# Performance work log

Measured on AMD Instinct MI355X. Metric: run time of the kernel, lower is better.

Reference implementation:

```python
import jax, jax.numpy as jnp
import numpy as np

BETA = 0.25


def setup_inputs() -> dict:
    key = jax.random.key(0)
    k1, k2 = jax.random.split(key)
    x = jax.random.normal(k1, (32, 512, 32, 32), dtype=jnp.float32)
    # torchhd Random embedding: random bipolar {-1,+1} hypervectors, non-trainable
    codebook = jnp.sign(jax.random.normal(k2, (1024, 512), dtype=jnp.float32))
    codebook = jnp.where(codebook == 0, 1.0, codebook)
    return {"x": x, "codebook": codebook}


def reference(x, codebook):
    B, C, W, H = x.shape
    K = codebook.shape[0]
    # training-mode path: sharp sigmoid soft-binarization -> [-1, 1]
    xs = jax.nn.sigmoid(x * 100.0) * 2.0 - 1.0
    # [B, C, W, H] -> [B*W*H, C]
    flat = jnp.transpose(xs, (0, 2, 3, 1)).reshape(-1, C)
    # squared-distance via norms + matmul (same expansion as the torch code)
    d = (
        jnp.sum(flat * flat, axis=1, keepdims=True)
        + jnp.sum(codebook * codebook, axis=1)
        - 2.0 * flat @ codebook.T
    )  # [N, K]
    indices = jnp.argmin(d, axis=1)  # [N]
    # perplexity from empirical code usage (unique+counts == bincount over present codes)
    counts = jnp.bincount(indices, length=K).astype(jnp.float32)
    n = jnp.asarray(indices.shape[0], dtype=jnp.float32)
    p = counts / n
    plogp = jnp.where(counts > 0, p * jnp.log(p), 0.0)
    entropy = -jnp.sum(plogp)
    perplexity = jnp.exp(entropy)
    perplexity_loss = 1.0 / perplexity
    loss = BETA * perplexity_loss
    # embedding gather + reshape back to [B, C, W, H]
    q = codebook[indices].reshape(B, W, H, C)
    q = jnp.transpose(q, (0, 3, 1, 2))
    # straight-through estimator
    quantized = xs + jax.lax.stop_gradient(q - xs)
    return quantized, perplexity_loss, loss
```

## Files before the change

### kernel.cpp

```cpp
#include <hip/hip_runtime.h>
#include <stdint.h>
#include <stddef.h>

#define CD 512
#define KC 1024
#define NR 32768

typedef __attribute__((ext_vector_type(8))) short short8_t;
typedef __attribute__((ext_vector_type(8))) __bf16 bf16x8_t;
typedef __attribute__((ext_vector_type(4))) float f32x4_t;

__device__ __forceinline__ uint16_t f2bf(float f) {
  uint32_t u = __float_as_uint(f);
  u += 0x7fffu + ((u >> 16) & 1u);
  return (uint16_t)(u >> 16);
}
__device__ __forceinline__ float bf2f(uint16_t h) {
  return __uint_as_float(((uint32_t)h) << 16);
}
__device__ __forceinline__ float soft_sign(float x) {
  float e = __expf(-100.0f * x);
  float s = __builtin_amdgcn_rcpf(1.0f + e);
  return fmaf(2.0f, s, -1.0f);
}

__global__ __launch_bounds__(256) void k_cb(const float* __restrict__ cb,
                                            uint16_t* __restrict__ cbb,
                                            uint32_t* __restrict__ pack) {
  int i = blockIdx.x * 256 + threadIdx.x;
  float v = cb[i];
  int k = i >> 9, c = i & 511;
  int cc = c & 63;
  int swz = ((((cc >> 3) ^ (k & 7)) << 3) | (cc & 7));
  cbb[((size_t)k << 9) + (c & ~63) + swz] = f2bf(v);
  unsigned long long m = __ballot(v > 0.0f);
  int lane = threadIdx.x & 63;
  if ((lane & 31) == 0) pack[((c >> 5) << 10) + k] = (uint32_t)(m >> (lane & 32));
}

__global__ __launch_bounds__(256) void k_prep(const float* __restrict__ x,
                                              uint16_t* __restrict__ xhi,
                                              uint16_t* __restrict__ xlo,
                                              float* __restrict__ srow) {
  __shared__ float lxs[64][129];
  int blk = blockIdx.x;
  int b = blk >> 3;
  int p0 = (blk & 7) << 7;
  int tid = threadIdx.x;
  int n0 = (b << 10) + p0;
  int oc = tid & 7, nr = tid >> 3;
  double sum[4] = {0.0, 0.0, 0.0, 0.0};
  const float* xb = x + (((size_t)b) << 19) + p0;

  for (int ch = 0; ch < 8; ++ch) {
    int c0 = ch << 6;
#pragma unroll
    for (int it = 0; it < 8; ++it) {
      int cr = (it << 3) + (tid >> 5);
      int q = tid & 31;
      const float4 v =
          *reinterpret_cast<const float4*>(xb + (((size_t)(c0 + cr)) << 10) + (q << 2));
      lxs[cr][(q << 2) + 0] = soft_sign(v.x);
      lxs[cr][(q << 2) + 1] = soft_sign(v.y);
      lxs[cr][(q << 2) + 2] = soft_sign(v.z);
      lxs[cr][(q << 2) + 3] = soft_sign(v.w);
    }
    __syncthreads();
#pragma unroll
    for (int it = 0; it < 4; ++it) {
      int r = (it << 5) + nr;
      int n = n0 + r;
      short8_t h8, l8;
      double ls = 0.0;
#pragma unroll
      for (int j = 0; j < 8; ++j) {
        float xs = lxs[(oc << 3) + j][r];
        uint16_t h = f2bf(xs);
        uint16_t l = f2bf(xs - bf2f(h));
        h8[j] = (short)h;
        l8[j] = (short)l;
        float sq = xs * xs;
        ls += (double)sq;
      }
      sum[it] += ls;
      size_t off = (((size_t)n) << 9) + (size_t)c0 + (size_t)(((oc ^ (n & 7)) << 3));
      *reinterpret_cast<short8_t*>(xhi + off) = h8;
      *reinterpret_cast<short8_t*>(xlo + off) = l8;
    }
    __syncthreads();
  }
#pragma unroll
  for (int it = 0; it < 4; ++it) {
    double s = sum[it];
#pragma unroll
    for (int m = 1; m < 8; m <<= 1) s += __shfl_xor(s, m);
    if (oc == 0) srow[n0 + (it << 5) + nr] = (float)s + 512.0f;
  }
}

__device__ __forceinline__ void gl_lds16(const uint16_t* g, uint16_t* l) {
  __builtin_amdgcn_global_load_lds((const uint32_t*)g, (uint32_t*)l, 16, 0, 0);
}

__global__ __launch_bounds__(512, 1) void k_gemm(
    const uint16_t* __restrict__ cbb, const uint16_t* __restrict__ xhi,
    const uint16_t* __restrict__ xlo, const float* __restrict__ srow,
    int* __restrict__ idx, int* __restrict__ counts) {
  extern __shared__ uint8_t smem[];
  uint16_t* lds = (uint16_t*)smem;

  int blk = blockIdx.x;
  int tid = threadIdx.x;
  int lane = tid & 63, wid = tid >> 6;
  int kg = wid >> 1, pg = wid & 1;
  int g = lane >> 4, r15 = lane & 15;
  int n0 = blk << 6;

  float s_p[2];
#pragma unroll
  for (int ac = 0; ac < 2; ++ac) s_p[ac] = srow[n0 + (pg << 5) + (ac << 4) + r15];

  float best_d[2];
  int best_k[2];
#pragma unroll
  for (int ac = 0; ac < 2; ++ac) { best_d[ac] = 3.4e38f; best_k[ac] = 0; }

  auto stageA = [&](int buf, int kt, int cc) {
    const uint16_t* base = cbb + ((size_t)(cc << 6)) + ((lane & 7) << 3);
    uint16_t* lb = lds + (buf << 13);
#pragma unroll
    for (int i = 0; i < 2; ++i) {
      int r = (wid << 1) + i;
      gl_lds16(base + (((size_t)((kt << 7) + (r << 3) + (lane >> 3))) << 9), lb + (r << 9));
    }
  };
  auto stageB = [&](int cc) {
#pragma unroll
    for (int t = 0; t < 2; ++t) {
      const uint16_t* src = t ? xlo : xhi;
      gl_lds16(src + (((size_t)(n0 + (wid << 3) + (lane >> 3))) << 9) + (cc << 6) +
                   ((lane & 7) << 3),
               lds + 16384 + (t << 15) + (cc << 12) + (wid << 9));
    }
  };

  f32x4_t acc[2][2];

  stageA(0, 0, 0);
  stageB(0);
  asm volatile("s_waitcnt vmcnt(0)" ::: "memory");
  __builtin_amdgcn_s_barrier();
  asm volatile("" ::: "memory");

  int cur = 0;
  for (int step = 0; step < 64; ++step) {
    int kt = step >> 3, cc = step & 7;
    if (cc == 0) {
#pragma unroll
      for (int i = 0; i < 2; ++i)
#pragma unroll
        for (int j = 0; j < 2; ++j) acc[i][j] = (f32x4_t){0.f, 0.f, 0.f, 0.f};
    }
    if (step < 7) stageB(step + 1);
    if (step < 63) {
      int ns = step + 1;
      stageA(cur ^ 1, ns >> 3, ns & 7);
    }

    const uint16_t* Acur = lds + (cur << 13);
    const uint16_t* Bc = lds + 16384 + (cc << 12);
#pragma unroll
    for (int cs = 0; cs < 2; ++cs) {
      bf16x8_t af[2], bh[2], bl[2];
#pragma unroll
      for (int ar = 0; ar < 2; ++ar) {
        int row = (kg << 5) + (ar << 4) + r15;
        int off = (row << 6) + (((((cs << 2) | g)) ^ (row & 7)) << 3);
        af[ar] = __builtin_bit_cast(bf16x8_t, *(const short8_t*)(Acur + off));
      }
#pragma unroll
      for (int ac = 0; ac < 2; ++ac) {
        int row = (pg << 5) + (ac << 4) + r15;
        int off = (row << 6) + ((((cs << 2) | g) ^ (row & 7)) << 3);
        bh[ac] = __builtin_bit_cast(bf16x8_t, *(const short8_t*)(Bc + off));
        bl[ac] = __builtin_bit_cast(bf16x8_t, *(const short8_t*)(Bc + 32768 + off));
      }
#pragma unroll
      for (int ar = 0; ar < 2; ++ar)
#pragma unroll
        for (int ac = 0; ac < 2; ++ac) {
          acc[ar][ac] =
              __builtin_amdgcn_mfma_f32_16x16x32_bf16(af[ar], bh[ac], acc[ar][ac], 0, 0, 0);
          acc[ar][ac] =
              __builtin_amdgcn_mfma_f32_16x16x32_bf16(af[ar], bl[ac], acc[ar][ac], 0, 0, 0);
        }
    }

    if (cc == 7) {
      int kbase = (kt << 7) + (kg << 5);
#pragma unroll
      for (int ar = 0; ar < 2; ++ar)
#pragma unroll
        for (int ac = 0; ac < 2; ++ac)
#pragma unroll
          for (int rg = 0; rg < 4; ++rg) {
            float d = fmaf(-2.0f, acc[ar][ac][rg], s_p[ac]);
            int kk = kbase + (ar << 4) + (g << 2) + rg;
            bool better = (d < best_d[ac]) || (d == best_d[ac] && kk < best_k[ac]);
            if (better) { best_d[ac] = d; best_k[ac] = kk; }
          }
    }

    asm volatile("s_waitcnt vmcnt(0)" ::: "memory");
    __builtin_amdgcn_s_barrier();
    asm volatile("" ::: "memory");
    cur ^= 1;
  }

  float rd0, rd1;
  int rk0, rk1;
  {
    float d = best_d[0];
    int k = best_k[0];
#pragma unroll
    for (int m = 16; m <= 32; m <<= 1) {
      float od = __shfl_xor(d, m);
      int ok = __shfl_xor(k, m);
      if (od < d || (od == d && ok < k)) { d = od; k = ok; }
    }
    rd0 = d; rk0 = k;
  }
  {
    float d = best_d[1];
    int k = best_k[1];
#pragma unroll
    for (int m = 16; m <= 32; m <<= 1) {
      float od = __shfl_xor(d, m);
      int ok = __shfl_xor(k, m);
      if (od < d || (od == d && ok < k)) { d = od; k = ok; }
    }
    rd1 = d; rk1 = k;
  }
  float* sd = (float*)smem;
  int* sk = (int*)(smem + 1024);
  __syncthreads();
  if (g < 2) {
    float dv = (g == 0) ? rd0 : rd1;
    int kv = (g == 0) ? rk0 : rk1;
    sd[(kg << 6) + (pg << 5) + (g << 4) + r15] = dv;
    sk[(kg << 6) + (pg << 5) + (g << 4) + r15] = kv;
  }
  __syncthreads();
  if (tid < 64) {
    float d0 = sd[tid];
    int k0 = sk[tid];
#pragma unroll
    for (int kgi = 1; kgi < 4; ++kgi) {
      float d1 = sd[(kgi << 6) + tid];
      int k1 = sk[(kgi << 6) + tid];
      if (d1 < d0 || (d1 == d0 && k1 < k0)) { d0 = d1; k0 = k1; }
    }
    idx[n0 + tid] = k0;
    atomicAdd(&counts[k0], 1);
  }
}

__global__ __launch_bounds__(256) void k_perp(const int* __restrict__ counts,
                                              float* __restrict__ out2) {
  int tid = threadIdx.x;
  float local = 0.0f;
  for (int i = tid; i < KC; i += 256) {
    int c = counts[i];
    if (c > 0) {
      float p = (float)c * (1.0f / 32768.0f);
      local += p * logf(p);
    }
  }
#pragma unroll
  for (int m = 1; m < 64; m <<= 1) local += __shfl_xor(local, m);
  __shared__ float wsum[4];
  if ((tid & 63) == 0) wsum[tid >> 6] = local;
  __syncthreads();
  if (tid == 0) {
    float entropy = -(wsum[0] + wsum[1] + wsum[2] + wsum[3]);
    float pl = 1.0f / expf(entropy);
    out2[0] = pl;
    out2[1] = 0.25f * pl;
  }
}

__global__ __launch_bounds__(256) void k_gather(const int* __restrict__ idx,
                                                const uint32_t* __restrict__ pack,
                                                float* __restrict__ out) {
  __shared__ uint32_t lp[16384];
  int tid = threadIdx.x;
#pragma unroll
  for (int i = 0; i < 16; ++i)
    reinterpret_cast<uint4*>(lp)[i * 256 + tid] =
        reinterpret_cast<const uint4*>(pack)[i * 256 + tid];
  __syncthreads();
  int base = blockIdx.x * 2048;
  for (int it = 0; it < 8; ++it) {
    int t = base + it * 256 + tid;
    int pq = t & 255;
    int c = (t >> 8) & 511;
    int b = t >> 17;
    int4 iv = reinterpret_cast<const int4*>(idx)[(b << 8) + pq];
    int cw = c >> 5, cbit = c & 31;
    float4 r;
    r.x = ((lp[(cw << 10) + iv.x] >> cbit) & 1) ? 1.0f : -1.0f;
    r.y = ((lp[(cw << 10) + iv.y] >> cbit) & 1) ? 1.0f : -1.0f;
    r.z = ((lp[(cw << 10) + iv.z] >> cbit) & 1) ? 1.0f : -1.0f;
    r.w = ((lp[(cw << 10) + iv.w] >> cbit) & 1) ? 1.0f : -1.0f;
    reinterpret_cast<float4*>(out)[t] = r;
  }
}

extern "C" void kernel_launch(void* const* d_in, const int* in_sizes, int n_in,
                              void* d_out, int out_size, void* d_ws, size_t ws_size,
                              hipStream_t stream) {
  (void)in_sizes; (void)n_in; (void)out_size;
  const float* x = (const float*)d_in[0];
  const float* cb = (const float*)d_in[1];
  float* out = (float*)d_out;

  uint8_t* ws = (uint8_t*)d_ws;
  uint16_t* cbb = (uint16_t*)ws;
  float* srow = (float*)(ws + 1048576);
  int* idx = (int*)(ws + 1048576 + 131072);
  int* counts = (int*)(ws + 1048576 + 131072 + 131072);
  uint32_t* pack = (uint32_t*)(ws + 1048576 + 131072 + 131072 + 4096);
  size_t small_end = 1048576 + 131072 + 131072 + 4096 + 65536;

  uint16_t *xhi, *xlo;
  if (ws_size >= small_end + (size_t)NR * CD * 2 * 2) {
    xhi = (uint16_t*)(ws + small_end);
    xlo = xhi + (size_t)NR * CD;
  } else {
    xhi = (uint16_t*)d_out;
    xlo = xhi + (size_t)NR * CD;
  }

  hipFuncSetAttribute((const void*)k_gemm, hipFuncAttributeMaxDynamicSharedMemorySize,
                      163840);

  k_cb<<<2048, 256, 0, stream>>>(cb, cbb, pack);
  k_prep<<<256, 256, 0, stream>>>(x, xhi, xlo, srow);
  hipMemsetAsync(counts, 0, 4096, stream);
  k_gemm<<<512, 512, 163840, stream>>>(cbb, xhi, xlo, srow, idx, counts);
  k_perp<<<1, 256, 0, stream>>>(counts, out + 16777216);
  k_gather<<<2048, 256, 0, stream>>>(idx, pack, out);
}
```

Baseline: 225.3 us.

## Fuse soft-sign preprocessing into GEMM kernel and retile codebook stages

```diff
diff --git a/kernel.cpp b/kernel.cpp
--- a/kernel.cpp
+++ b/kernel.cpp
@@ -29,177 +29,143 @@
                                             uint32_t* __restrict__ pack) {
   int i = blockIdx.x * 256 + threadIdx.x;
   float v = cb[i];
+  cbb[i] = f2bf(v);
   int k = i >> 9, c = i & 511;
-  int cc = c & 63;
-  int swz = ((((cc >> 3) ^ (k & 7)) << 3) | (cc & 7));
-  cbb[((size_t)k << 9) + (c & ~63) + swz] = f2bf(v);
   unsigned long long m = __ballot(v > 0.0f);
   int lane = threadIdx.x & 63;
   if ((lane & 31) == 0) pack[((c >> 5) << 10) + k] = (uint32_t)(m >> (lane & 32));
 }
 
-__global__ __launch_bounds__(256) void k_prep(const float* __restrict__ x,
-                                              uint16_t* __restrict__ xhi,
-                                              uint16_t* __restrict__ xlo,
-                                              float* __restrict__ srow) {
-  __shared__ float lxs[64][129];
-  int blk = blockIdx.x;
-  int b = blk >> 3;
-  int p0 = (blk & 7) << 7;
-  int tid = threadIdx.x;
-  int n0 = (b << 10) + p0;
-  int oc = tid & 7, nr = tid >> 3;
-  double sum[4] = {0.0, 0.0, 0.0, 0.0};
+__device__ __forceinline__ void gl_lds16(const uint16_t* g, uint16_t* l) {
+  __builtin_amdgcn_global_load_lds((const uint32_t*)g, (uint32_t*)l, 16, 0, 0);
+}
+
+__global__ __launch_bounds__(512, 1) void k_gemm(const uint16_t* __restrict__ cbb,
+                                                 const float* __restrict__ x,
+                                                 int* __restrict__ idx,
+                                                 int* __restrict__ counts) {
+  extern __shared__ uint8_t smem[];
+  uint16_t* lds = (uint16_t*)smem;
+
+  const int tid = threadIdx.x;
+  const int lane = tid & 63, wid = tid >> 6;
+  const int kg = wid >> 1, pg = wid & 1;
+  const int g = lane >> 4, r15 = lane & 15;
+  const int blk = blockIdx.x;
+  const int n0 = blk << 6;
+  const int b = blk >> 4, p0 = (blk & 15) << 6;
+
+  auto stageA = [&](int buf, int kt, int cc) {
+    uint16_t* dst = lds + (buf << 13);
+    const uint16_t* srcb = cbb + ((size_t)(kt << 8)) * 512 + (cc << 5);
+#pragma unroll
+    for (int i = 0; i < 2; ++i) {
+      int u = (i << 9) + tid;
+      gl_lds16(srcb + (size_t)(u >> 2) * 512 + ((u & 3) << 3), dst + (u << 3));
+    }
+  };
+  stageA(0, 0, 0);
+
+  float* raw = (float*)(smem + 16384);
   const float* xb = x + (((size_t)b) << 19) + p0;
-
+  const int fr = tid >> 3, foc = tid & 7;
+  double nsum = 0.0;
   for (int ch = 0; ch < 8; ++ch) {
     int c0 = ch << 6;
 #pragma unroll
-    for (int it = 0; it < 8; ++it) {
-      int cr = (it << 3) + (tid >> 5);
-      int q = tid & 31;
+    for (int it = 0; it < 2; ++it) {
+      int u = (it << 9) + tid;
+      int cr = u >> 4, q = u & 15;
       const float4 v =
-          *reinterpret_cast<const float4*>(xb + (((size_t)(c0 + cr)) << 10) + (q << 2));
-      lxs[cr][(q << 2) + 0] = soft_sign(v.x);
-      lxs[cr][(q << 2) + 1] = soft_sign(v.y);
-      lxs[cr][(q << 2) + 2] = soft_sign(v.z);
-      lxs[cr][(q << 2) + 3] = soft_sign(v.w);
+          *reinterpret_cast<const float4*>(xb + (size_t)(c0 + cr) * 1024 + (q << 2));
+      *reinterpret_cast<float4*>(raw + (cr << 6) +
+                                 ((q << 2) ^ ((((cr >> 3) & 7)) << 2))) = v;
     }
     __syncthreads();
-#pragma unroll
-    for (int it = 0; it < 4; ++it) {
-      int r = (it << 5) + nr;
-      int n = n0 + r;
-      short8_t h8, l8;
-      double ls = 0.0;
-#pragma unroll
-      for (int j = 0; j < 8; ++j) {
-        float xs = lxs[(oc << 3) + j][r];
-        uint16_t h = f2bf(xs);
-        uint16_t l = f2bf(xs - bf2f(h));
-        h8[j] = (short)h;
-        l8[j] = (short)l;
-        float sq = xs * xs;
-        ls += (double)sq;
-      }
-      sum[it] += ls;
-      size_t off = (((size_t)n) << 9) + (size_t)c0 + (size_t)(((oc ^ (n & 7)) << 3));
-      *reinterpret_cast<short8_t*>(xhi + off) = h8;
-      *reinterpret_cast<short8_t*>(xlo + off) = l8;
-    }
+    short8_t h8, l8;
+    double ls = 0.0;
+#pragma unroll
+    for (int j = 0; j < 8; ++j) {
+      int c = (foc << 3) + j;
+      float xs = soft_sign(raw[(c << 6) + (fr ^ (foc << 2))]);
+      uint16_t h = f2bf(xs);
+      uint16_t l = f2bf(xs - bf2f(h));
+      h8[j] = (short)h;
+      l8[j] = (short)l;
+      float sq = xs * xs;
+      ls += (double)sq;
+    }
+    nsum += ls;
+    int cc = (ch << 1) + (foc >> 2), jj = foc & 3;
+    uint16_t* bwp = (uint16_t*)(smem + 32768 + (cc << 12)) + (fr << 5) + (jj << 3);
+    *reinterpret_cast<short8_t*>(bwp) = h8;
+    *reinterpret_cast<short8_t*>(bwp + 32768) = l8;
     __syncthreads();
   }
-#pragma unroll
-  for (int it = 0; it < 4; ++it) {
-    double s = sum[it];
-#pragma unroll
-    for (int m = 1; m < 8; m <<= 1) s += __shfl_xor(s, m);
-    if (oc == 0) srow[n0 + (it << 5) + nr] = (float)s + 512.0f;
-  }
-}
-
-__device__ __forceinline__ void gl_lds16(const uint16_t* g, uint16_t* l) {
-  __builtin_amdgcn_global_load_lds((const uint32_t*)g, (uint32_t*)l, 16, 0, 0);
-}
-
-__global__ __launch_bounds__(512, 1) void k_gemm(
-    const uint16_t* __restrict__ cbb, const uint16_t* __restrict__ xhi,
-    const uint16_t* __restrict__ xlo, const float* __restrict__ srow,
-    int* __restrict__ idx, int* __restrict__ counts) {
-  extern __shared__ uint8_t smem[];
-  uint16_t* lds = (uint16_t*)smem;
-
-  int blk = blockIdx.x;
-  int tid = threadIdx.x;
-  int lane = tid & 63, wid = tid >> 6;
-  int kg = wid >> 1, pg = wid & 1;
-  int g = lane >> 4, r15 = lane & 15;
-  int n0 = blk << 6;
-
+  {
+    double s = nsum;
+    s += __shfl_xor(s, 1);
+    s += __shfl_xor(s, 2);
+    s += __shfl_xor(s, 4);
+    if (foc == 0) ((float*)raw)[fr] = (float)s + 512.0f;
+  }
+  __syncthreads();
   float s_p[2];
 #pragma unroll
-  for (int ac = 0; ac < 2; ++ac) s_p[ac] = srow[n0 + (pg << 5) + (ac << 4) + r15];
+  for (int ac = 0; ac < 2; ++ac) s_p[ac] = ((float*)raw)[(pg << 5) + (ac << 4) + r15];
+  __syncthreads();
 
   float best_d[2];
   int best_k[2];
 #pragma unroll
   for (int ac = 0; ac < 2; ++ac) { best_d[ac] = 3.4e38f; best_k[ac] = 0; }
 
-  auto stageA = [&](int buf, int kt, int cc) {
-    const uint16_t* base = cbb + ((size_t)(cc << 6)) + ((lane & 7) << 3);
-    uint16_t* lb = lds + (buf << 13);
-#pragma unroll
-    for (int i = 0; i < 2; ++i) {
-      int r = (wid << 1) + i;
-      gl_lds16(base + (((size_t)((kt << 7) + (r << 3) + (lane >> 3))) << 9), lb + (r << 9));
-    }
-  };
-  auto stageB = [&](int cc) {
-#pragma unroll
-    for (int t = 0; t < 2; ++t) {
-      const uint16_t* src = t ? xlo : xhi;
-      gl_lds16(src + (((size_t)(n0 + (wid << 3) + (lane >> 3))) << 9) + (cc << 6) +
-                   ((lane & 7) << 3),
-               lds + 16384 + (t << 15) + (cc << 12) + (wid << 9));
-    }
-  };
-
-  f32x4_t acc[2][2];
-
-  stageA(0, 0, 0);
-  stageB(0);
-  asm volatile("s_waitcnt vmcnt(0)" ::: "memory");
-  __builtin_amdgcn_s_barrier();
-  asm volatile("" ::: "memory");
-
+  f32x4_t acc[4][2];
   int cur = 0;
   for (int step = 0; step < 64; ++step) {
-    int kt = step >> 3, cc = step & 7;
+    int kt = step >> 4, cc = step & 15;
     if (cc == 0) {
 #pragma unroll
-      for (int i = 0; i < 2; ++i)
+      for (int i = 0; i < 4; ++i)
 #pragma unroll
         for (int j = 0; j < 2; ++j) acc[i][j] = (f32x4_t){0.f, 0.f, 0.f, 0.f};
     }
-    if (step < 7) stageB(step + 1);
     if (step < 63) {
       int ns = step + 1;
-      stageA(cur ^ 1, ns >> 3, ns & 7);
-    }
-
-    const uint16_t* Acur = lds + (cur << 13);
-    const uint16_t* Bc = lds + 16384 + (cc << 12);
-#pragma unroll
-    for (int cs = 0; cs < 2; ++cs) {
-      bf16x8_t af[2], bh[2], bl[2];
-#pragma unroll
-      for (int ar = 0; ar < 2; ++ar) {
-        int row = (kg << 5) + (ar << 4) + r15;
-        int off = (row << 6) + (((((cs << 2) | g)) ^ (row & 7)) << 3);
-        af[ar] = __builtin_bit_cast(bf16x8_t, *(const short8_t*)(Acur + off));
+      stageA(cur ^ 1, ns >> 4, ns & 15);
+    }
+
+    const uint16_t* A = lds + (cur << 13);
+    const uint16_t* Bh = (uint16_t*)(smem + 32768) + (cc << 11);
+    bf16x8_t af[4], fbh[2], fbl[2];
+#pragma unroll
+    for (int ar = 0; ar < 4; ++ar) {
+      int row = (kg << 6) + (ar << 4) + r15;
+      af[ar] = __builtin_bit_cast(bf16x8_t,
+                                  *(const short8_t*)(A + (row << 5) + (g << 3)));
+    }
+#pragma unroll
+    for (int ac = 0; ac < 2; ++ac) {
+      int row = (pg << 5) + (ac << 4) + r15;
+      fbh[ac] = __builtin_bit_cast(bf16x8_t,
+                                   *(const short8_t*)(Bh + (row << 5) + (g << 3)));
+      fbl[ac] = __builtin_bit_cast(
+          bf16x8_t, *(const short8_t*)(Bh + 32768 + (row << 5) + (g << 3)));
+    }
+#pragma unroll
+    for (int ar = 0; ar < 4; ++ar)
+#pragma unroll
+      for (int ac = 0; ac < 2; ++ac) {
+        acc[ar][ac] =
+            __builtin_amdgcn_mfma_f32_16x16x32_bf16(af[ar], fbh[ac], acc[ar][ac], 0, 0, 0);
+        acc[ar][ac] =
+            __builtin_amdgcn_mfma_f32_16x16x32_bf16(af[ar], fbl[ac], acc[ar][ac], 0, 0, 0);
       }
-#pragma unroll
-      for (int ac = 0; ac < 2; ++ac) {
-        int row = (pg << 5) + (ac << 4) + r15;
-        int off = (row << 6) + ((((cs << 2) | g) ^ (row & 7)) << 3);
-        bh[ac] = __builtin_bit_cast(bf16x8_t, *(const short8_t*)(Bc + off));
-        bl[ac] = __builtin_bit_cast(bf16x8_t, *(const short8_t*)(Bc + 32768 + off));
-      }
-#pragma unroll
-      for (int ar = 0; ar < 2; ++ar)
-#pragma unroll
-        for (int ac = 0; ac < 2; ++ac) {
-          acc[ar][ac] =
-              __builtin_amdgcn_mfma_f32_16x16x32_bf16(af[ar], bh[ac], acc[ar][ac], 0, 0, 0);
-          acc[ar][ac] =
-              __builtin_amdgcn_mfma_f32_16x16x32_bf16(af[ar], bl[ac], acc[ar][ac], 0, 0, 0);
-        }
-    }
-
-    if (cc == 7) {
-      int kbase = (kt << 7) + (kg << 5);
-#pragma unroll
-      for (int ar = 0; ar < 2; ++ar)
+
+    if (cc == 15) {
+      int kbase = (kt << 8) + (kg << 6);
+#pragma unroll
+      for (int ar = 0; ar < 4; ++ar)
 #pragma unroll
         for (int ac = 0; ac < 2; ++ac)
 #pragma unroll
@@ -319,35 +285,23 @@
 extern "C" void kernel_launch(void* const* d_in, const int* in_sizes, int n_in,
                               void* d_out, int out_size, void* d_ws, size_t ws_size,
                               hipStream_t stream) {
-  (void)in_sizes; (void)n_in; (void)out_size;
+  (void)in_sizes; (void)n_in; (void)out_size; (void)ws_size;
   const float* x = (const float*)d_in[0];
   const float* cb = (const float*)d_in[1];
   float* out = (float*)d_out;
 
   uint8_t* ws = (uint8_t*)d_ws;
   uint16_t* cbb = (uint16_t*)ws;
-  float* srow = (float*)(ws + 1048576);
-  int* idx = (int*)(ws + 1048576 + 131072);
-  int* counts = (int*)(ws + 1048576 + 131072 + 131072);
-  uint32_t* pack = (uint32_t*)(ws + 1048576 + 131072 + 131072 + 4096);
-  size_t small_end = 1048576 + 131072 + 131072 + 4096 + 65536;
-
-  uint16_t *xhi, *xlo;
-  if (ws_size >= small_end + (size_t)NR * CD * 2 * 2) {
-    xhi = (uint16_t*)(ws + small_end);
-    xlo = xhi + (size_t)NR * CD;
-  } else {
-    xhi = (uint16_t*)d_out;
-    xlo = xhi + (size_t)NR * CD;
-  }
+  int* idx = (int*)(ws + 1048576);
+  int* counts = (int*)(ws + 1048576 + 131072);
+  uint32_t* pack = (uint32_t*)(ws + 1048576 + 131072 + 4096);
 
   hipFuncSetAttribute((const void*)k_gemm, hipFuncAttributeMaxDynamicSharedMemorySize,
                       163840);
 
   k_cb<<<2048, 256, 0, stream>>>(cb, cbb, pack);
-  k_prep<<<256, 256, 0, stream>>>(x, xhi, xlo, srow);
   hipMemsetAsync(counts, 0, 4096, stream);
-  k_gemm<<<512, 512, 163840, stream>>>(cbb, xhi, xlo, srow, idx, counts);
+  k_gemm<<<512, 512, 163840, stream>>>(cbb, x, idx, counts);
   k_perp<<<1, 256, 0, stream>>>(counts, out + 16777216);
   k_gather<<<2048, 256, 0, stream>>>(idx, pack, out);
 }
```

After: 213.9 us. -5.0%, faster.
